# Performance work log

Hardware: AMD Instinct MI355X
Metric: run time of the kernel (lower is better)

## Reference

```python
import jax, jax.numpy as jnp
import numpy as np

B, C, L, H = 4, 512, 2048, 8
DH = C // H
SCALE = DH ** -0.5
EPS = 1e-5  # torch LayerNorm default


def setup_inputs() -> dict:
    key = jax.random.key(0)
    ks = jax.random.split(key, 3)
    x = jax.random.normal(ks[0], (B, C, L), dtype=jnp.float32)
    # Conv1d kernel_size=1 == per-position linear; weights ~ N(0, 1/C)
    w_qkv = jax.random.normal(ks[1], (3 * C, C), dtype=jnp.float32) / np.sqrt(C)
    b_qkv = jnp.zeros((3 * C,), dtype=jnp.float32)
    # NOTE: original uses zero_module(proj_out); random weights used here so the
    # baseline is non-trivial for kernel correctness testing.
    w_proj = jax.random.normal(ks[2], (C, C), dtype=jnp.float32) / np.sqrt(C)
    b_proj = jnp.zeros((C,), dtype=jnp.float32)
    ln_gamma = jnp.ones((C,), dtype=jnp.float32)
    ln_beta = jnp.zeros((C,), dtype=jnp.float32)
    return {"x": x, "ln_gamma": ln_gamma, "ln_beta": ln_beta,
            "w_qkv": w_qkv, "b_qkv": b_qkv, "w_proj": w_proj, "b_proj": b_proj}


def reference(x, ln_gamma, ln_beta, w_qkv, b_qkv, w_proj, b_proj):
    # ChannelNorm: LayerNorm over channel dim. Work in [B, L, C] layout.
    h = jnp.swapaxes(x, 1, 2)                      # [B, L, C]
    mu = jnp.mean(h, axis=-1, keepdims=True)
    var = jnp.mean((h - mu) ** 2, axis=-1, keepdims=True)
    hn = (h - mu) * jax.lax.rsqrt(var + EPS) * ln_gamma + ln_beta

    # QKV 1x1 conv as GEMM: [B, L, 3C]
    qkv = jnp.einsum('blc,dc->bld', hn, w_qkv) + b_qkv
    qkv = qkv.reshape(B, L, 3, H, DH)
    q, k, v = (qkv[:, :, i].transpose(0, 2, 1, 3) for i in range(3))  # [B, H, L, DH]

    # Scaled dot-product attention (full O(L^2) scores, as in source)
    w = jnp.einsum('bhqd,bhkd->bhqk', q, k) * SCALE
    w = jax.nn.softmax(w, axis=-1)
    o = jnp.einsum('bhqk,bhkd->bhqd', w, v)        # [B, H, L, DH]
    o = o.transpose(0, 2, 1, 3).reshape(B, L, C)

    # proj_out 1x1 conv + residual (dropout in eval mode = identity)
    out = jnp.einsum('blc,dc->bld', o, w_proj) + b_proj
    return jnp.swapaxes(out, 1, 2) + x             # [B, C, L]
```

## Files before the change

kernel.cpp:

```cpp
#include <hip/hip_runtime.h>
#include <hip/hip_bf16.h>

typedef __bf16 bf16;
typedef bf16 bf16x8 __attribute__((ext_vector_type(8)));
typedef bf16 bf16x4 __attribute__((ext_vector_type(4)));
typedef float f32x4 __attribute__((ext_vector_type(4)));

constexpr int B = 4, C = 512, L = 2048, H = 8, DH = 64;
constexpr int BL = B * L;
constexpr int BH = B * H;
constexpr int N_QKV = 3 * C;
constexpr float QSCALE = 0.125f * 1.44269504088896f;
constexpr float EPS = 1e-5f;

constexpr size_t SZ = (size_t)BL * C;
constexpr size_t OFF_HN    = 0;
constexpr size_t OFF_WQKV  = OFF_HN    + SZ * 2;
constexpr size_t OFF_WPROJ = OFF_WQKV  + (size_t)N_QKV * C * 2;
constexpr size_t OFF_Q     = OFF_WPROJ + (size_t)C * C * 2;
constexpr size_t OFF_K     = OFF_Q     + SZ * 2;
constexpr size_t OFF_V     = OFF_K     + SZ * 2;
constexpr size_t OFF_O     = OFF_V     + SZ * 2;
constexpr size_t OFF_STATS = OFF_O     + SZ * 2;
constexpr size_t OFF_OPART = OFF_STATS + (size_t)BL * 2 * 4;
constexpr size_t OFF_ML    = OFF_OPART + (size_t)2 * BH * L * DH * 2;

__device__ __forceinline__ bf16x8 ld8(const bf16* p) {
  return *(const bf16x8*)p;
}

__device__ __forceinline__ void gll16(const bf16* g, bf16* l) {
  __builtin_amdgcn_global_load_lds(
      (const __attribute__((address_space(1))) unsigned int*)(const void*)g,
      (__attribute__((address_space(3))) unsigned int*)(void*)l, 16, 0, 0);
}

__device__ __forceinline__ unsigned pack_bf16(float a, float b) {
  unsigned ua = __builtin_bit_cast(unsigned, a) + 0x8000u;
  unsigned ub = __builtin_bit_cast(unsigned, b) + 0x8000u;
  return __builtin_amdgcn_perm(ub, ua, 0x07060302u);
}
__device__ __forceinline__ float bf_lo(unsigned u) { return __builtin_bit_cast(float, u << 16); }
__device__ __forceinline__ float bf_hi(unsigned u) { return __builtin_bit_cast(float, u & 0xFFFF0000u); }

__global__ __launch_bounds__(1024) void k_ln(const float* __restrict__ x,
                                             const float* __restrict__ gamma,
                                             const float* __restrict__ beta,
                                             const float* __restrict__ wqkv,
                                             const float* __restrict__ wproj,
                                             bf16* __restrict__ hn,
                                             bf16* __restrict__ wqkv_b,
                                             bf16* __restrict__ wproj_b) {
  int blk = blockIdx.x;
  int b = blk >> 6;
  int l0 = (blk & 63) << 5;
  int t = threadIdx.x;
  int ll = t & 31;
  int cg = t >> 5;
  __shared__ float tile[512][33];
  __shared__ float sh_s[32][33];
  __shared__ float sh_q[32][33];
  __shared__ float mu_s[32], rs_s[32];
  const float* xp = x + ((size_t)b * C) * L + l0;
  float s = 0.f, ss = 0.f;
#pragma unroll
  for (int r = 0; r < 16; ++r) {
    int c = cg * 16 + r;
    float v = xp[(size_t)c * L + ll];
    tile[c][ll] = v;
    s += v; ss += v * v;
  }
  sh_s[cg][ll] = s; sh_q[cg][ll] = ss;
  __syncthreads();
  if (t < 32) {
    float ts = 0.f, tq = 0.f;
#pragma unroll
    for (int i = 0; i < 32; ++i) { ts += sh_s[i][t]; tq += sh_q[i][t]; }
    float mu = ts * (1.0f / C);
    float var = tq * (1.0f / C) - mu * mu;
    mu_s[t] = mu;
    rs_s[t] = rsqrtf(var + EPS);
  }
  __syncthreads();
  int c2 = (t & 255) * 2;
  int lgrp = t >> 8;
  float g0 = gamma[c2], g1 = gamma[c2 + 1];
  float b0 = beta[c2],  b1 = beta[c2 + 1];
#pragma unroll
  for (int it = 0; it < 8; ++it) {
    int l = lgrp * 8 + it;
    float mu = mu_s[l], rstd = rs_s[l];
    float v0 = (tile[c2][l]     - mu) * rstd * g0 + b0;
    float v1 = (tile[c2 + 1][l] - mu) * rstd * g1 + b1;
    *(unsigned*)&hn[(size_t)(b * L + l0 + l) * C + c2] = pack_bf16(v0, v1);
  }
  int gid = blk * 1024 + t;
#pragma unroll
  for (int i = 0; i < 3; ++i)
    wqkv_b[gid + i * 262144] = (bf16)wqkv[gid + i * 262144];
  wproj_b[gid] = (bf16)wproj[gid];
}

__global__ __launch_bounds__(256) void k_gemm_qkv(const bf16* __restrict__ hn,
                                                  const bf16* __restrict__ wq,
                                                  const float* __restrict__ bq,
                                                  bf16* __restrict__ qg,
                                                  bf16* __restrict__ kg,
                                                  bf16* __restrict__ vg) {
  int mt = blockIdx.x, nt = blockIdx.y;
  int m0 = mt << 7, n0 = nt << 7;
  int t = threadIdx.x, lane = t & 63, w = t >> 6;
  int mw = w >> 1, nw = w & 1;
  int q4 = lane >> 4, c16 = lane & 15;
  __shared__ __align__(16) char smem[36864];
  bf16* As = (bf16*)smem;
  bf16* Bs = (bf16*)(smem + 16384);

  int goff[4], ldsoff[4];
#pragma unroll
  for (int p = 0; p < 4; ++p) {
    int idx = (p * 4 + w) * 64 + lane;
    int row = idx >> 3, s0 = idx & 7;
    goff[p] = row * C + (s0 ^ (row & 7)) * 8;
    ldsoff[p] = (p * 4 + w) * 512;
  }

  f32x4 acc[4][4];
#pragma unroll
  for (int mi = 0; mi < 4; ++mi)
#pragma unroll
    for (int ni = 0; ni < 4; ++ni) acc[mi][ni] = (f32x4){0.f, 0.f, 0.f, 0.f};

  const bf16* ap = hn + (size_t)m0 * C;
  const bf16* bp = wq + (size_t)n0 * C;
  for (int k0 = 0; k0 < C; k0 += 64) {
    __syncthreads();
#pragma unroll
    for (int p = 0; p < 4; ++p) {
      gll16(ap + k0 + goff[p], As + ldsoff[p]);
      gll16(bp + k0 + goff[p], Bs + ldsoff[p]);
    }
    __syncthreads();
#pragma unroll
    for (int kk2 = 0; kk2 < 2; ++kk2) {
      bf16x8 af[4], bfr[4];
#pragma unroll
      for (int mi = 0; mi < 4; ++mi) {
        int row = mw * 64 + mi * 16 + c16;
        af[mi] = ld8(As + row * 64 + ((kk2 * 4 + q4) ^ (row & 7)) * 8);
      }
#pragma unroll
      for (int ni = 0; ni < 4; ++ni) {
        int row = nw * 64 + ni * 16 + c16;
        bfr[ni] = ld8(Bs + row * 64 + ((kk2 * 4 + q4) ^ (row & 7)) * 8);
      }
#pragma unroll
      for (int mi = 0; mi < 4; ++mi)
#pragma unroll
        for (int ni = 0; ni < 4; ++ni)
          acc[mi][ni] = __builtin_amdgcn_mfma_f32_16x16x32_bf16(af[mi], bfr[ni], acc[mi][ni], 0, 0, 0);
    }
  }
  __syncthreads();

  int i = nt >> 2;
  int h = ((nt & 3) << 1) + nw;
  int b = m0 >> 11;
  int l0 = (m0 & (L - 1)) + mw * 64;
  float bias[4];
#pragma unroll
  for (int ni = 0; ni < 4; ++ni) bias[ni] = bq[n0 + nw * 64 + ni * 16 + c16];
  bf16* Os = (bf16*)(smem + w * 9216);

  if (i == 2) {
#pragma unroll
    for (int mi = 0; mi < 4; ++mi)
#pragma unroll
      for (int ni = 0; ni < 4; ++ni) {
        bf16x4 pk;
#pragma unroll
        for (int r = 0; r < 4; ++r) pk[r] = (bf16)(acc[mi][ni][r] + bias[ni]);
        *(bf16x4*)&Os[(ni * 16 + c16) * 72 + mi * 16 + q4 * 4] = pk;
      }
    __syncthreads();
    const bf16* src = Os + lane * 72;
    bf16* dst = vg + ((size_t)((b * H + h) * DH + lane)) * L + l0;
#pragma unroll
    for (int s = 0; s < 8; ++s)
      *(uint4*)(dst + s * 8) = *(const uint4*)(src + s * 8);
  } else {
    float sc = (i == 0) ? QSCALE : 1.0f;
#pragma unroll
    for (int mi = 0; mi < 4; ++mi)
#pragma unroll
      for (int ni = 0; ni < 4; ++ni)
#pragma unroll
        for (int r = 0; r < 4; ++r)
          Os[(mi * 16 + q4 * 4 + r) * 72 + ni * 16 + c16] = (bf16)((acc[mi][ni][r] + bias[ni]) * sc);
    __syncthreads();
    bf16* dst0 = (i == 0) ? qg : kg;
    const bf16* src = Os + lane * 72;
    bf16* dst = dst0 + ((size_t)((b * H + h) * L + l0 + lane)) * DH;
#pragma unroll
    for (int s = 0; s < 8; ++s)
      *(uint4*)(dst + s * 8) = *(const uint4*)(src + s * 8);
  }
}

__global__ __launch_bounds__(256, 4) void k_attn(const bf16* __restrict__ qg,
                                                 const bf16* __restrict__ kg,
                                                 const bf16* __restrict__ vt,
                                                 bf16* __restrict__ opart,
                                                 float* __restrict__ lsum) {
  int blk = blockIdx.x;
  int js = blk & 1; blk >>= 1;
  int qt = blk & 15; int bh = blk >> 4;
  int t = threadIdx.x, lane = t & 63, w = t >> 6;
  int q4 = lane >> 4, c16 = lane & 15;
  __shared__ __align__(16) bf16 Ks[64][64];
  __shared__ __align__(16) bf16 Vts[64][64];
  __shared__ __align__(16) bf16 Ps[4][16][72];
  const bf16* qptr  = qg + ((size_t)bh * L + qt * 128 + w * 32) * DH;
  const bf16* kptr  = kg + (size_t)bh * L * DH;
  const bf16* vtptr = vt + (size_t)bh * DH * L;

  int ksoff[2], vsoff[2];
#pragma unroll
  for (int p = 0; p < 2; ++p) {
    int ci = p * 256 + w * 64 + lane;
    int row = ci >> 3, s0 = ci & 7;
    int ch = s0 ^ (row & 7);
    ksoff[p] = row * DH + ch * 8;
    vsoff[p] = row * L + ch * 8;
  }
  int sw = c16 & 7;

  bf16x8 qf[2][2];
#pragma unroll
  for (int qb = 0; qb < 2; ++qb)
#pragma unroll
    for (int kk2 = 0; kk2 < 2; ++kk2)
      qf[qb][kk2] = ld8(&qptr[(size_t)(qb * 16 + c16) * DH + kk2 * 32 + q4 * 8]);

  f32x4 o_acc[2][4];
  float l_i[2] = {0.f, 0.f};
#pragma unroll
  for (int qb = 0; qb < 2; ++qb)
#pragma unroll
    for (int db = 0; db < 4; ++db) o_acc[qb][db] = (f32x4){0.f, 0.f, 0.f, 0.f};

  for (int j0 = js * 1024; j0 < js * 1024 + 1024; j0 += 64) {
    __syncthreads();
#pragma unroll
    for (int p = 0; p < 2; ++p) {
      gll16(kptr + (size_t)j0 * DH + ksoff[p], &Ks[0][0]  + (p * 4 + w) * 512);
      gll16(vtptr + j0 + vsoff[p],             &Vts[0][0] + (p * 4 + w) * 512);
    }
    __syncthreads();

    f32x4 s[2][4];
#pragma unroll
    for (int qb = 0; qb < 2; ++qb)
#pragma unroll
      for (int jb = 0; jb < 4; ++jb) s[qb][jb] = (f32x4){0.f, 0.f, 0.f, 0.f};
#pragma unroll
    for (int kk2 = 0; kk2 < 2; ++kk2) {
      int choff = ((kk2 * 4 + q4) ^ sw) * 8;
#pragma unroll
      for (int jb = 0; jb < 4; ++jb) {
        bf16x8 kf = ld8(&Ks[0][0] + (jb * 16 + c16) * 64 + choff);
        s[0][jb] = __builtin_amdgcn_mfma_f32_16x16x32_bf16(kf, qf[0][kk2], s[0][jb], 0, 0, 0);
        s[1][jb] = __builtin_amdgcn_mfma_f32_16x16x32_bf16(kf, qf[1][kk2], s[1][jb], 0, 0, 0);
      }
    }

#pragma unroll
    for (int qb = 0; qb < 2; ++qb) {
      float rs = 0.f;
#pragma unroll
      for (int jb = 0; jb < 4; ++jb)
#pragma unroll
        for (int r = 0; r < 4; ++r) {
          float p_ = __builtin_amdgcn_exp2f(s[qb][jb][r]);
          s[qb][jb][r] = p_;
          rs += p_;
        }
      l_i[qb] += rs;
    }

    bf16x8 vf[2][4];
#pragma unroll
    for (int kk2 = 0; kk2 < 2; ++kk2) {
      int choff = ((kk2 * 4 + q4) ^ sw) * 8;
#pragma unroll
      for (int db = 0; db < 4; ++db)
        vf[kk2][db] = ld8(&Vts[0][0] + (db * 16 + c16) * 64 + choff);
    }

#pragma unroll
    for (int qb = 0; qb < 2; ++qb) {
#pragma unroll
      for (int jb = 0; jb < 4; ++jb) {
        uint2 pk;
        pk.x = pack_bf16(s[qb][jb][0], s[qb][jb][1]);
        pk.y = pack_bf16(s[qb][jb][2], s[qb][jb][3]);
        *(uint2*)&Ps[w][c16][jb * 16 + q4 * 4] = pk;
      }
#pragma unroll
      for (int kk2 = 0; kk2 < 2; ++kk2) {
        bf16x8 pf = ld8(&Ps[w][c16][kk2 * 32 + q4 * 8]);
#pragma unroll
        for (int db = 0; db < 4; ++db)
          o_acc[qb][db] = __builtin_amdgcn_mfma_f32_16x16x32_bf16(vf[kk2][db], pf, o_acc[qb][db], 0, 0, 0);
      }
    }
  }

#pragma unroll
  for (int qb = 0; qb < 2; ++qb) {
    float lf = l_i[qb];
    lf += __shfl_xor(lf, 16, 64);
    lf += __shfl_xor(lf, 32, 64);
    int q = qt * 128 + w * 32 + qb * 16 + c16;
    bf16* op = opart + (((size_t)js * BH + bh) * L + q) * DH;
#pragma unroll
    for (int db = 0; db < 4; ++db) {
      uint2 pk;
      pk.x = pack_bf16(o_acc[qb][db][0], o_acc[qb][db][1]);
      pk.y = pack_bf16(o_acc[qb][db][2], o_acc[qb][db][3]);
      *(uint2*)&op[db * 16 + q4 * 4] = pk;
    }
    if (q4 == 0) lsum[((size_t)js * BH + bh) * L + q] = lf;
  }
}

__global__ __launch_bounds__(256) void k_gemm_proj(const bf16* __restrict__ opart,
                                                   const float* __restrict__ lsum,
                                                   const bf16* __restrict__ wp,
                                                   const float* __restrict__ bp,
                                                   const float* __restrict__ x,
                                                   float* __restrict__ out) {
  int mt = blockIdx.x, nt = blockIdx.y;
  int m0 = mt << 6, n0 = nt << 6;
  int t = threadIdx.x;
  int lane = t & 63, w = t >> 6;
  int q4 = lane >> 4, c16 = lane & 15;
  __shared__ __align__(16) bf16 As[64][72];
  __shared__ __align__(16) bf16 Bs[64][72];
  __shared__ float Ot[64][65];
  __shared__ float invs[64][9];
  int b = m0 >> 11, q0 = m0 & (L - 1);
  for (int i = t; i < 512; i += 256) {
    int row = i >> 3, h = i & 7;
    int bhh = b * 8 + h;
    float l0v = lsum[(size_t)bhh * L + q0 + row];
    float l1v = lsum[((size_t)BH + bhh) * L + q0 + row];
    invs[row][h] = 1.0f / (l0v + l1v);
  }
  f32x4 acc[4];
#pragma unroll
  for (int nb = 0; nb < 4; ++nb) acc[nb] = (f32x4){0.f, 0.f, 0.f, 0.f};

  for (int k0 = 0; k0 < C; k0 += 64) {
    __syncthreads();
    int h = k0 >> 6;
    const bf16* ap0 = opart + ((size_t)(b * 8 + h) * L + q0) * 64;
    const bf16* ap1 = opart + ((size_t)(BH + b * 8 + h) * L + q0) * 64;
#pragma unroll
    for (int p = 0; p < 2; ++p) {
      int idx = p * 256 + t;
      int row = idx >> 3, ch = idx & 7;
      uint4 u0 = *(const uint4*)(ap0 + (size_t)row * 64 + ch * 8);
      uint4 u1 = *(const uint4*)(ap1 + (size_t)row * 64 + ch * 8);
      float inv = invs[row][h];
      unsigned* pu0 = (unsigned*)&u0;
      unsigned* pu1 = (unsigned*)&u1;
      uint4 m;
      unsigned* pm = (unsigned*)&m;
#pragma unroll
      for (int k = 0; k < 4; ++k)
        pm[k] = pack_bf16((bf_lo(pu0[k]) + bf_lo(pu1[k])) * inv,
                          (bf_hi(pu0[k]) + bf_hi(pu1[k])) * inv);
      *(uint4*)&As[row][ch * 8] = m;
      *(bf16x8*)&Bs[row][ch * 8] = ld8(&wp[(size_t)(n0 + row) * C + k0 + ch * 8]);
    }
    __syncthreads();
#pragma unroll
    for (int kk = 0; kk < 64; kk += 32) {
      bf16x8 a = ld8(&As[w * 16 + c16][kk + q4 * 8]);
#pragma unroll
      for (int nb = 0; nb < 4; ++nb) {
        bf16x8 bfr = ld8(&Bs[nb * 16 + c16][kk + q4 * 8]);
        acc[nb] = __builtin_amdgcn_mfma_f32_16x16x32_bf16(a, bfr, acc[nb], 0, 0, 0);
      }
    }
  }
  __syncthreads();
#pragma unroll
  for (int nb = 0; nb < 4; ++nb)
#pragma unroll
    for (int r = 0; r < 4; ++r)
      Ot[w * 16 + q4 * 4 + r][nb * 16 + c16] = acc[nb][r];
  __syncthreads();
#pragma unroll
  for (int r = 0; r < 16; ++r) {
    int cl = w * 16 + r;
    int c = n0 + cl;
    size_t idx = (size_t)(b * C + c) * L + q0 + lane;
    out[idx] = Ot[lane][cl] + bp[c] + x[idx];
  }
}

extern "C" void kernel_launch(void* const* d_in, const int* in_sizes, int n_in,
                              void* d_out, int out_size, void* d_ws, size_t ws_size,
                              hipStream_t stream) {
  const float* x     = (const float*)d_in[0];
  const float* gamma = (const float*)d_in[1];
  const float* beta  = (const float*)d_in[2];
  const float* wqkv  = (const float*)d_in[3];
  const float* bqkv  = (const float*)d_in[4];
  const float* wproj = (const float*)d_in[5];
  const float* bproj = (const float*)d_in[6];
  float* out = (float*)d_out;
  char* ws = (char*)d_ws;
  bf16* hn  = (bf16*)(ws + OFF_HN);
  bf16* wqb = (bf16*)(ws + OFF_WQKV);
  bf16* wpb = (bf16*)(ws + OFF_WPROJ);
  bf16* qbp = (bf16*)(ws + OFF_Q);
  bf16* kbp = (bf16*)(ws + OFF_K);
  bf16* vbp = (bf16*)(ws + OFF_V);
  bf16* opart = (bf16*)(ws + OFF_OPART);
  float* lsum = (float*)(ws + OFF_ML);

  hipLaunchKernelGGL(k_ln, dim3(B * (L / 32)), dim3(1024), 0, stream,
                     x, gamma, beta, wqkv, wproj, hn, wqb, wpb);
  hipLaunchKernelGGL(k_gemm_qkv, dim3(BL / 128, N_QKV / 128), dim3(256), 0, stream,
                     hn, wqb, bqkv, qbp, kbp, vbp);
  hipLaunchKernelGGL(k_attn, dim3(B * H * (L / 128) * 2), dim3(256), 0, stream,
                     qbp, kbp, vbp, opart, lsum);
  hipLaunchKernelGGL(k_gemm_proj, dim3(BL / 64, C / 64), dim3(256), 0, stream,
                     opart, lsum, wpb, bproj, x, out);
}
```

Measured before the change: 171.8 us.

## Double-buffer K/V tiles in attention with async prefetch and swizzled P buffer

Attention's K and V^T LDS tiles become double-buffered, so the next 64-key tile is prefetched with direct global-to-LDS loads while the current tile is computed, with manual vmcnt waits and raw barriers replacing the paired __syncthreads. V fragment loads are hoisted ahead of the softmax exponentials. The P staging buffer drops its padding for an XOR swizzle to avoid bank conflicts, and s_setprio brackets the MFMA sections. The cost is twice the K/V LDS footprint, which may lower occupancy, plus fragile hand-written wait counts.

Result: slower. 212.9 us (+23.9%).

```diff
diff --git a/kernel.cpp b/kernel.cpp
--- a/kernel.cpp
+++ b/kernel.cpp
@@ -217,9 +217,9 @@
   int qt = blk & 15; int bh = blk >> 4;
   int t = threadIdx.x, lane = t & 63, w = t >> 6;
   int q4 = lane >> 4, c16 = lane & 15;
-  __shared__ __align__(16) bf16 Ks[64][64];
-  __shared__ __align__(16) bf16 Vts[64][64];
-  __shared__ __align__(16) bf16 Ps[4][16][72];
+  __shared__ __align__(16) bf16 Ks[2][64][64];
+  __shared__ __align__(16) bf16 Vts[2][64][64];
+  __shared__ __align__(16) bf16 Ps[4][16][64];
   const bf16* qptr  = qg + ((size_t)bh * L + qt * 128 + w * 32) * DH;
   const bf16* kptr  = kg + (size_t)bh * L * DH;
   const bf16* vtptr = vt + (size_t)bh * DH * L;
@@ -234,6 +234,7 @@
     vsoff[p] = row * L + ch * 8;
   }
   int sw = c16 & 7;
+  int psw = (c16 & 7) << 1;
 
   bf16x8 qf[2][2];
 #pragma unroll
@@ -249,29 +250,58 @@
 #pragma unroll
     for (int db = 0; db < 4; ++db) o_acc[qb][db] = (f32x4){0.f, 0.f, 0.f, 0.f};
 
-  for (int j0 = js * 1024; j0 < js * 1024 + 1024; j0 += 64) {
-    __syncthreads();
+  {
+    int j0 = js * 1024;
 #pragma unroll
     for (int p = 0; p < 2; ++p) {
-      gll16(kptr + (size_t)j0 * DH + ksoff[p], &Ks[0][0]  + (p * 4 + w) * 512);
-      gll16(vtptr + j0 + vsoff[p],             &Vts[0][0] + (p * 4 + w) * 512);
-    }
-    __syncthreads();
+      gll16(kptr + (size_t)j0 * DH + ksoff[p], &Ks[0][0][0]  + (p * 4 + w) * 512);
+      gll16(vtptr + j0 + vsoff[p],             &Vts[0][0][0] + (p * 4 + w) * 512);
+    }
+  }
+
+  for (int it = 0; it < 16; ++it) {
+    int cur = it & 1;
+    if (it < 15) {
+      int j1 = js * 1024 + (it + 1) * 64;
+#pragma unroll
+      for (int p = 0; p < 2; ++p) {
+        gll16(kptr + (size_t)j1 * DH + ksoff[p], &Ks[cur ^ 1][0][0]  + (p * 4 + w) * 512);
+        gll16(vtptr + j1 + vsoff[p],             &Vts[cur ^ 1][0][0] + (p * 4 + w) * 512);
+      }
+      asm volatile("s_waitcnt vmcnt(4)" ::: "memory");
+    } else {
+      asm volatile("s_waitcnt vmcnt(0)" ::: "memory");
+    }
+    __builtin_amdgcn_s_barrier();
+    __builtin_amdgcn_sched_barrier(0);
+    const bf16* KsC = &Ks[cur][0][0];
+    const bf16* VsC = &Vts[cur][0][0];
 
     f32x4 s[2][4];
 #pragma unroll
     for (int qb = 0; qb < 2; ++qb)
 #pragma unroll
       for (int jb = 0; jb < 4; ++jb) s[qb][jb] = (f32x4){0.f, 0.f, 0.f, 0.f};
+    __builtin_amdgcn_s_setprio(1);
 #pragma unroll
     for (int kk2 = 0; kk2 < 2; ++kk2) {
       int choff = ((kk2 * 4 + q4) ^ sw) * 8;
 #pragma unroll
       for (int jb = 0; jb < 4; ++jb) {
-        bf16x8 kf = ld8(&Ks[0][0] + (jb * 16 + c16) * 64 + choff);
+        bf16x8 kf = ld8(KsC + (jb * 16 + c16) * 64 + choff);
         s[0][jb] = __builtin_amdgcn_mfma_f32_16x16x32_bf16(kf, qf[0][kk2], s[0][jb], 0, 0, 0);
         s[1][jb] = __builtin_amdgcn_mfma_f32_16x16x32_bf16(kf, qf[1][kk2], s[1][jb], 0, 0, 0);
       }
+    }
+    __builtin_amdgcn_s_setprio(0);
+
+    bf16x8 vf[2][4];
+#pragma unroll
+    for (int kk2 = 0; kk2 < 2; ++kk2) {
+      int choff = ((kk2 * 4 + q4) ^ sw) * 8;
+#pragma unroll
+      for (int db = 0; db < 4; ++db)
+        vf[kk2][db] = ld8(VsC + (db * 16 + c16) * 64 + choff);
     }
 
 #pragma unroll
@@ -288,15 +318,6 @@
       l_i[qb] += rs;
     }
 
-    bf16x8 vf[2][4];
-#pragma unroll
-    for (int kk2 = 0; kk2 < 2; ++kk2) {
-      int choff = ((kk2 * 4 + q4) ^ sw) * 8;
-#pragma unroll
-      for (int db = 0; db < 4; ++db)
-        vf[kk2][db] = ld8(&Vts[0][0] + (db * 16 + c16) * 64 + choff);
-    }
-
 #pragma unroll
     for (int qb = 0; qb < 2; ++qb) {
 #pragma unroll
@@ -304,16 +325,20 @@
         uint2 pk;
         pk.x = pack_bf16(s[qb][jb][0], s[qb][jb][1]);
         pk.y = pack_bf16(s[qb][jb][2], s[qb][jb][3]);
-        *(uint2*)&Ps[w][c16][jb * 16 + q4 * 4] = pk;
-      }
+        *(uint2*)&Ps[w][c16][((jb * 4 + q4) ^ psw) * 4] = pk;
+      }
+      __builtin_amdgcn_s_setprio(1);
 #pragma unroll
       for (int kk2 = 0; kk2 < 2; ++kk2) {
-        bf16x8 pf = ld8(&Ps[w][c16][kk2 * 32 + q4 * 8]);
+        bf16x8 pf = ld8(&Ps[w][c16][((kk2 * 8 + q4 * 2) ^ psw) * 4]);
 #pragma unroll
         for (int db = 0; db < 4; ++db)
           o_acc[qb][db] = __builtin_amdgcn_mfma_f32_16x16x32_bf16(vf[kk2][db], pf, o_acc[qb][db], 0, 0, 0);
       }
-    }
+      __builtin_amdgcn_s_setprio(0);
+    }
+    __builtin_amdgcn_sched_barrier(0);
+    __builtin_amdgcn_s_barrier();
   }
 
 #pragma unroll
```

## Shrink attention query tile to 64 rows and remap blocks for XCD locality

Applied to the files above, without the earlier changes.

Halves the per-wave query tile from 32 to 16 rows, doubling the attention grid and raising launch bounds to 8 blocks per CU so register pressure drops and occupancy rises. Block indices are remapped so that consecutive block IDs, taken 8 at a time, cover 8 different bh heads, and all 64 query/split blocks of a given head share one residue mod 8. This is apparently meant to keep K/V reuse local to one XCD's cache. The P scratch buffer is shrunk and XOR-swizzled, and the P/V MFMA now runs per 32-key chunk, with V fragments loaded inline. The trade-off is that each K/V tile is reloaded into LDS by twice as many blocks, which lowers reuse per load.

Result: slower. 187.8 us (+9.3%).

```diff
diff --git a/kernel.cpp b/kernel.cpp
--- a/kernel.cpp
+++ b/kernel.cpp
@@ -207,20 +207,23 @@
   }
 }
 
-__global__ __launch_bounds__(256, 4) void k_attn(const bf16* __restrict__ qg,
+__global__ __launch_bounds__(256, 8) void k_attn(const bf16* __restrict__ qg,
                                                  const bf16* __restrict__ kg,
                                                  const bf16* __restrict__ vt,
                                                  bf16* __restrict__ opart,
                                                  float* __restrict__ lsum) {
-  int blk = blockIdx.x;
-  int js = blk & 1; blk >>= 1;
-  int qt = blk & 15; int bh = blk >> 4;
+  int i0 = blockIdx.x;
+  int x = i0 & 7, slot = i0 >> 3;
+  int bh = ((slot >> 6) << 3) + x;
+  int inner = slot & 63;
+  int js = inner >> 5;
+  int qt = inner & 31;
   int t = threadIdx.x, lane = t & 63, w = t >> 6;
   int q4 = lane >> 4, c16 = lane & 15;
   __shared__ __align__(16) bf16 Ks[64][64];
   __shared__ __align__(16) bf16 Vts[64][64];
-  __shared__ __align__(16) bf16 Ps[4][16][72];
-  const bf16* qptr  = qg + ((size_t)bh * L + qt * 128 + w * 32) * DH;
+  __shared__ __align__(16) bf16 Ps[4][16][32];
+  const bf16* qptr  = qg + ((size_t)bh * L + qt * 64 + w * 16) * DH;
   const bf16* kptr  = kg + (size_t)bh * L * DH;
   const bf16* vtptr = vt + (size_t)bh * DH * L;
 
@@ -234,22 +237,20 @@
     vsoff[p] = row * L + ch * 8;
   }
   int sw = c16 & 7;
-
-  bf16x8 qf[2][2];
-#pragma unroll
-  for (int qb = 0; qb < 2; ++qb)
-#pragma unroll
-    for (int kk2 = 0; kk2 < 2; ++kk2)
-      qf[qb][kk2] = ld8(&qptr[(size_t)(qb * 16 + c16) * DH + kk2 * 32 + q4 * 8]);
-
-  f32x4 o_acc[2][4];
-  float l_i[2] = {0.f, 0.f};
-#pragma unroll
-  for (int qb = 0; qb < 2; ++qb)
-#pragma unroll
-    for (int db = 0; db < 4; ++db) o_acc[qb][db] = (f32x4){0.f, 0.f, 0.f, 0.f};
-
-  for (int j0 = js * 1024; j0 < js * 1024 + 1024; j0 += 64) {
+  int psw = (c16 & 3) << 1;
+
+  bf16x8 qf[2];
+#pragma unroll
+  for (int kk2 = 0; kk2 < 2; ++kk2)
+    qf[kk2] = ld8(&qptr[(size_t)c16 * DH + kk2 * 32 + q4 * 8]);
+
+  f32x4 o_acc[4];
+  float l_i = 0.f;
+#pragma unroll
+  for (int db = 0; db < 4; ++db) o_acc[db] = (f32x4){0.f, 0.f, 0.f, 0.f};
+
+  for (int it = 0; it < 16; ++it) {
+    int j0 = js * 1024 + it * 64;
     __syncthreads();
 #pragma unroll
     for (int p = 0; p < 2; ++p) {
@@ -258,76 +259,63 @@
     }
     __syncthreads();
 
-    f32x4 s[2][4];
-#pragma unroll
-    for (int qb = 0; qb < 2; ++qb)
-#pragma unroll
-      for (int jb = 0; jb < 4; ++jb) s[qb][jb] = (f32x4){0.f, 0.f, 0.f, 0.f};
+    f32x4 s[4];
+#pragma unroll
+    for (int jb = 0; jb < 4; ++jb) s[jb] = (f32x4){0.f, 0.f, 0.f, 0.f};
 #pragma unroll
     for (int kk2 = 0; kk2 < 2; ++kk2) {
       int choff = ((kk2 * 4 + q4) ^ sw) * 8;
 #pragma unroll
       for (int jb = 0; jb < 4; ++jb) {
         bf16x8 kf = ld8(&Ks[0][0] + (jb * 16 + c16) * 64 + choff);
-        s[0][jb] = __builtin_amdgcn_mfma_f32_16x16x32_bf16(kf, qf[0][kk2], s[0][jb], 0, 0, 0);
-        s[1][jb] = __builtin_amdgcn_mfma_f32_16x16x32_bf16(kf, qf[1][kk2], s[1][jb], 0, 0, 0);
-      }
-    }
-
-#pragma unroll
-    for (int qb = 0; qb < 2; ++qb) {
+        s[jb] = __builtin_amdgcn_mfma_f32_16x16x32_bf16(kf, qf[kk2], s[jb], 0, 0, 0);
+      }
+    }
+
+    {
       float rs = 0.f;
 #pragma unroll
       for (int jb = 0; jb < 4; ++jb)
 #pragma unroll
         for (int r = 0; r < 4; ++r) {
-          float p_ = __builtin_amdgcn_exp2f(s[qb][jb][r]);
-          s[qb][jb][r] = p_;
+          float p_ = __builtin_amdgcn_exp2f(s[jb][r]);
+          s[jb][r] = p_;
           rs += p_;
         }
-      l_i[qb] += rs;
-    }
-
-    bf16x8 vf[2][4];
+      l_i += rs;
+    }
+
 #pragma unroll
     for (int kk2 = 0; kk2 < 2; ++kk2) {
       int choff = ((kk2 * 4 + q4) ^ sw) * 8;
 #pragma unroll
-      for (int db = 0; db < 4; ++db)
-        vf[kk2][db] = ld8(&Vts[0][0] + (db * 16 + c16) * 64 + choff);
-    }
-
-#pragma unroll
-    for (int qb = 0; qb < 2; ++qb) {
-#pragma unroll
-      for (int jb = 0; jb < 4; ++jb) {
+      for (int jbl = 0; jbl < 2; ++jbl) {
+        int jb = kk2 * 2 + jbl;
         uint2 pk;
-        pk.x = pack_bf16(s[qb][jb][0], s[qb][jb][1]);
-        pk.y = pack_bf16(s[qb][jb][2], s[qb][jb][3]);
-        *(uint2*)&Ps[w][c16][jb * 16 + q4 * 4] = pk;
-      }
-#pragma unroll
-      for (int kk2 = 0; kk2 < 2; ++kk2) {
-        bf16x8 pf = ld8(&Ps[w][c16][kk2 * 32 + q4 * 8]);
-#pragma unroll
-        for (int db = 0; db < 4; ++db)
-          o_acc[qb][db] = __builtin_amdgcn_mfma_f32_16x16x32_bf16(vf[kk2][db], pf, o_acc[qb][db], 0, 0, 0);
-      }
-    }
-  }
-
-#pragma unroll
-  for (int qb = 0; qb < 2; ++qb) {
-    float lf = l_i[qb];
+        pk.x = pack_bf16(s[jb][0], s[jb][1]);
+        pk.y = pack_bf16(s[jb][2], s[jb][3]);
+        *(uint2*)&Ps[w][c16][((jbl * 4 + q4) ^ psw) * 4] = pk;
+      }
+      bf16x8 pf = ld8(&Ps[w][c16][((q4 * 2) ^ psw) * 4]);
+#pragma unroll
+      for (int db = 0; db < 4; ++db) {
+        bf16x8 vfr = ld8(&Vts[0][0] + (db * 16 + c16) * 64 + choff);
+        o_acc[db] = __builtin_amdgcn_mfma_f32_16x16x32_bf16(vfr, pf, o_acc[db], 0, 0, 0);
+      }
+    }
+  }
+
+  {
+    float lf = l_i;
     lf += __shfl_xor(lf, 16, 64);
     lf += __shfl_xor(lf, 32, 64);
-    int q = qt * 128 + w * 32 + qb * 16 + c16;
+    int q = qt * 64 + w * 16 + c16;
     bf16* op = opart + (((size_t)js * BH + bh) * L + q) * DH;
 #pragma unroll
     for (int db = 0; db < 4; ++db) {
       uint2 pk;
-      pk.x = pack_bf16(o_acc[qb][db][0], o_acc[qb][db][1]);
-      pk.y = pack_bf16(o_acc[qb][db][2], o_acc[qb][db][3]);
+      pk.x = pack_bf16(o_acc[db][0], o_acc[db][1]);
+      pk.y = pack_bf16(o_acc[db][2], o_acc[db][3]);
       *(uint2*)&op[db * 16 + q4 * 4] = pk;
     }
     if (q4 == 0) lsum[((size_t)js * BH + bh) * L + q] = lf;
@@ -436,7 +424,7 @@
                      x, gamma, beta, wqkv, wproj, hn, wqb, wpb);
   hipLaunchKernelGGL(k_gemm_qkv, dim3(BL / 128, N_QKV / 128), dim3(256), 0, stream,
                      hn, wqb, bqkv, qbp, kbp, vbp);
-  hipLaunchKernelGGL(k_attn, dim3(B * H * (L / 128) * 2), dim3(256), 0, stream,
+  hipLaunchKernelGGL(k_attn, dim3(B * H * (L / 64) * 2), dim3(256), 0, stream,
                      qbp, kbp, vbp, opart, lsum);
   hipLaunchKernelGGL(k_gemm_proj, dim3(BL / 64, C / 64), dim3(256), 0, stream,
                      opart, lsum, wpb, bproj, x, out);
```
